# Performance work log

Measured on AMD Instinct MI355X. Metric: run time of the kernel, lower is better.

## Reference

```python
import jax, jax.numpy as jnp
import numpy as np
from jax import lax

NPOINT = 2048
RADIUS = 0.1
NSAMPLE = 32


def setup_inputs() -> dict:
    key = jax.random.key(0)
    ks = jax.random.split(key, 6)
    B, N, C = 8, 16384, 16
    xyz = jax.random.uniform(ks[0], (B, N, 3), dtype=jnp.float32)
    features = jax.random.normal(ks[1], (B, N, C), dtype=jnp.float32)
    W1 = jax.random.normal(ks[2], (C, 32), dtype=jnp.float32) * 0.1
    b1 = jnp.zeros((32,), jnp.float32)
    W2 = jax.random.normal(ks[3], (32, 32), dtype=jnp.float32) * 0.1
    b2 = jnp.zeros((32,), jnp.float32)
    W3 = jax.random.normal(ks[4], (32, 64), dtype=jnp.float32) * 0.1
    b3 = jnp.zeros((64,), jnp.float32)
    return {"xyz": xyz, "features": features,
            "W1": W1, "b1": b1, "W2": W2, "b2": b2, "W3": W3, "b3": b3}


def farthest_point_sample(xyz, npoint):
    # Sequential FPS: keep running min-distance to selected set, argmax each step.
    B, N, _ = xyz.shape

    def step(carry, _):
        min_d, far = carry  # min_d: [B,N], far: [B]
        centroid = jnp.take_along_axis(xyz, far[:, None, None], axis=1)  # [B,1,3]
        d = jnp.sum((xyz - centroid) ** 2, axis=-1)                      # [B,N]
        min_d = jnp.minimum(min_d, d)
        nxt = jnp.argmax(min_d, axis=1).astype(jnp.int32)
        return (min_d, nxt), far

    init = (jnp.full((B, N), 1e10, xyz.dtype), jnp.zeros((B,), jnp.int32))
    _, idx = lax.scan(step, init, None, length=npoint)  # idx: [npoint, B]
    return idx.T  # [B, npoint]


def ball_query(radius, nsample, xyz, new_xyz):
    # Squared pairwise distances [B, S, N]
    d2 = (jnp.sum(new_xyz ** 2, -1)[:, :, None]
          + jnp.sum(xyz ** 2, -1)[:, None, :]
          - 2.0 * jnp.einsum('bsd,bnd->bsn', new_xyz, xyz))
    N = xyz.shape[1]
    # Take the first `nsample` in-ball indices (by point order), pad with first found.
    scores = jnp.where(d2 <= radius * radius,
                       jnp.arange(N, dtype=jnp.int32), jnp.int32(N))
    vals = -lax.top_k(-scores, nsample)[0]  # smallest nsample scores, ascending
    first = vals[..., :1]                   # center itself is always in-ball
    return jnp.where(vals == N, first, vals)  # [B, S, nsample] int32


def reference(xyz, features, W1, b1, W2, b2, W3, b3):
    fps_idx = farthest_point_sample(xyz, NPOINT)                      # [B,S]
    new_xyz = jnp.take_along_axis(xyz, fps_idx[..., None], axis=1)    # [B,S,3]
    idx = ball_query(RADIUS, NSAMPLE, xyz, new_xyz)                   # [B,S,K]
    grouped = jax.vmap(lambda f, i: f[i])(features, idx)              # [B,S,K,C]
    h = jax.nn.relu(grouped @ W1 + b1)
    h = jax.nn.relu(h @ W2 + b2)
    h = h @ W3 + b3                                                   # [B,S,K,64]
    new_features = jnp.max(h, axis=2)                                 # [B,S,64]
    return new_xyz, new_features
```

## Files before the change

kernel.cpp:

```cpp
#include <hip/hip_runtime.h>

#define B 8
#define N 16384
#define S 2048
#define NS 32
#define CIN 16
#define NCELL 4096

typedef float f32x2 __attribute__((ext_vector_type(2)));
typedef int   i32x2 __attribute__((ext_vector_type(2)));
typedef unsigned long long u64;

template<int CTRL>
__device__ __forceinline__ float dpp_fmax(float x) {
    int t = __builtin_amdgcn_update_dpp(0, __float_as_int(x), CTRL, 0xF, 0xF, true);
    return fmaxf(x, __int_as_float(t));
}
template<int CTRL>
__device__ __forceinline__ unsigned dpp_umax(unsigned x) {
    unsigned t = (unsigned)__builtin_amdgcn_update_dpp(0, (int)x, CTRL, 0xF, 0xF, true);
    return x > t ? x : t;
}
__device__ __forceinline__ float wave_fmax(float x) {
    x = dpp_fmax<0xB1>(x);
    x = dpp_fmax<0x4E>(x);
    x = dpp_fmax<0x114>(x);
    x = dpp_fmax<0x118>(x);
    x = dpp_fmax<0x142>(x);
    x = dpp_fmax<0x143>(x);
    return __int_as_float(__builtin_amdgcn_readlane(__float_as_int(x), 63));
}
__device__ __forceinline__ unsigned wave_umax(unsigned x) {
    x = dpp_umax<0xB1>(x);
    x = dpp_umax<0x4E>(x);
    x = dpp_umax<0x114>(x);
    x = dpp_umax<0x118>(x);
    x = dpp_umax<0x142>(x);
    x = dpp_umax<0x143>(x);
    return (unsigned)__builtin_amdgcn_readlane((int)x, 63);
}

__device__ __forceinline__ int expand4(int v) {
    return (v & 1) | ((v & 2) << 2) | ((v & 4) << 4) | ((v & 8) << 6);
}

__global__ __launch_bounds__(1024) void bucket_kernel(const float* __restrict__ xyz,
                                                      float* __restrict__ Xp,
                                                      float* __restrict__ Yp,
                                                      float* __restrict__ Zp,
                                                      int* __restrict__ Ip) {
    const int b = blockIdx.x;
    const int t = threadIdx.x;
    const float* xb = xyz + (size_t)b * N * 3;

    __shared__ int hist[NCELL];
    __shared__ int run[NCELL];
    __shared__ int pA[1024], pB[1024];
    for (int i = t; i < NCELL; i += 1024) { hist[i] = 0; run[i] = 0; }
    __syncthreads();

    int cell[16];
    float xs[16], ys[16], zs[16];
#pragma unroll
    for (int k = 0; k < 16; ++k) {
        const int n = t + (k << 10);
        const float x = xb[3 * n + 0];
        const float y = xb[3 * n + 1];
        const float z = xb[3 * n + 2];
        const int cx = min(15, max(0, (int)(x * 16.0f)));
        const int cy = min(15, max(0, (int)(y * 16.0f)));
        const int cz = min(15, max(0, (int)(z * 16.0f)));
        const int c = expand4(cx) | (expand4(cy) << 1) | (expand4(cz) << 2);
        cell[k] = c; xs[k] = x; ys[k] = y; zs[k] = z;
        atomicAdd(&hist[c], 1);
    }
    __syncthreads();

    const int h0 = hist[4 * t + 0], h1 = hist[4 * t + 1],
              h2 = hist[4 * t + 2], h3 = hist[4 * t + 3];
    const int lsum = h0 + h1 + h2 + h3;
    pA[t] = lsum;
    __syncthreads();
    int* cur = pA; int* nxt = pB;
    for (int off = 1; off < 1024; off <<= 1) {
        nxt[t] = cur[t] + ((t >= off) ? cur[t - off] : 0);
        __syncthreads();
        int* tmp = cur; cur = nxt; nxt = tmp;
    }
    const int excl = cur[t] - lsum;
    __syncthreads();
    hist[4 * t + 0] = excl;
    hist[4 * t + 1] = excl + h0;
    hist[4 * t + 2] = excl + h0 + h1;
    hist[4 * t + 3] = excl + h0 + h1 + h2;
    __syncthreads();

#pragma unroll
    for (int k = 0; k < 16; ++k) {
        const int c = cell[k];
        const int pos = hist[c] + atomicAdd(&run[c], 1);
        const size_t o = (size_t)b * N + pos;
        Xp[o] = xs[k]; Yp[o] = ys[k]; Zp[o] = zs[k];
        Ip[o] = t + (k << 10);
    }
}

__global__ __launch_bounds__(1024, 1) void fps_prune_kernel(const float* __restrict__ xyz,
                                                            const float* __restrict__ Xp,
                                                            const float* __restrict__ Yp,
                                                            const float* __restrict__ Zp,
                                                            const int* __restrict__ Ip,
                                                            float* __restrict__ new_xyz) {
#pragma clang fp contract(off)
    const int b = blockIdx.x;
    const int t = threadIdx.x;
    const float* xb = xyz + (size_t)b * N * 3;
    const size_t base = (size_t)b * N + ((size_t)t << 4);

    f32x2 px[8], py[8], pz[8], md[8];
    i32x2 ip[8];
    {
        const f32x2* X2 = (const f32x2*)(Xp + base);
        const f32x2* Y2 = (const f32x2*)(Yp + base);
        const f32x2* Z2 = (const f32x2*)(Zp + base);
        const i32x2* I2 = (const i32x2*)(Ip + base);
#pragma unroll
        for (int j = 0; j < 8; ++j) {
            px[j] = X2[j]; py[j] = Y2[j]; pz[j] = Z2[j]; ip[j] = I2[j];
            md[j] = (f32x2){1e10f, 1e10f};
        }
    }

    float lox = px[0].x, hix = px[0].x, loy = py[0].x, hiy = py[0].x,
          loz = pz[0].x, hiz = pz[0].x;
#pragma unroll
    for (int j = 0; j < 8; ++j) {
        lox = fminf(lox, fminf(px[j].x, px[j].y)); hix = fmaxf(hix, fmaxf(px[j].x, px[j].y));
        loy = fminf(loy, fminf(py[j].x, py[j].y)); hiy = fmaxf(hiy, fmaxf(py[j].x, py[j].y));
        loz = fminf(loz, fminf(pz[j].x, pz[j].y)); hiz = fmaxf(hiz, fmaxf(pz[j].x, pz[j].y));
    }

    __shared__ u64 slotp[4];
    if (t == 0) { slotp[0] = 0ull; slotp[1] = 0ull; slotp[2] = 0ull; slotp[3] = 0ull; }
    __syncthreads();

    int p = 0;
    float ub = 1e10f;
    int cand = ip[0].x;
    u64 wkey = 0ull;
    float cx = xb[0], cy = xb[1], cz = xb[2];

    for (int it = 0; it < S; ++it) {
        if (t == 0) {
            float* o = new_xyz + ((size_t)b * S + it) * 3;
            o[0] = cx; o[1] = cy; o[2] = cz;
        }
        const float ddx = fmaxf(0.0f, fmaxf(lox - cx, cx - hix));
        const float ddy = fmaxf(0.0f, fmaxf(loy - cy, cy - hiy));
        const float ddz = fmaxf(0.0f, fmaxf(loz - cz, cz - hiz));
        const float lb = (ddx * ddx + ddy * ddy) + ddz * ddz;
        const bool upd = !(lb * 0.99998f > ub);

        if (__any(upd)) {
            if (upd) {
                asm volatile("" : "+v"(px[0]), "+v"(px[1]), "+v"(px[2]), "+v"(px[3]),
                                  "+v"(px[4]), "+v"(px[5]), "+v"(px[6]), "+v"(px[7]));
                asm volatile("" : "+v"(py[0]), "+v"(py[1]), "+v"(py[2]), "+v"(py[3]),
                                  "+v"(py[4]), "+v"(py[5]), "+v"(py[6]), "+v"(py[7]));
                asm volatile("" : "+v"(pz[0]), "+v"(pz[1]), "+v"(pz[2]), "+v"(pz[3]),
                                  "+v"(pz[4]), "+v"(pz[5]), "+v"(pz[6]), "+v"(pz[7]));
                asm volatile("" : "+v"(ip[0]), "+v"(ip[1]), "+v"(ip[2]), "+v"(ip[3]),
                                  "+v"(ip[4]), "+v"(ip[5]), "+v"(ip[6]), "+v"(ip[7]));
                const f32x2 c2x = {cx, cx}, c2y = {cy, cy}, c2z = {cz, cz};
                f32x2 nu2 = {0.0f, 0.0f};
#pragma unroll
                for (int j = 0; j < 8; ++j) {
                    const f32x2 dx = px[j] - c2x;
                    const f32x2 dy = py[j] - c2y;
                    const f32x2 dz = pz[j] - c2z;
                    const f32x2 dd = (dx * dx + dy * dy) + dz * dz;
                    const f32x2 m = __builtin_elementwise_min(md[j], dd);
                    md[j] = m;
                    nu2 = __builtin_elementwise_max(nu2, m);
                }
                const float nu = fmaxf(nu2.x, nu2.y);
                int c = 0x7fffffff;
#pragma unroll
                for (int j = 0; j < 8; ++j) {
                    if (md[j].x == nu) c = min(c, ip[j].x);
                    if (md[j].y == nu) c = min(c, ip[j].y);
                }
                ub = nu; cand = c;
            }
            const float wmax = wave_fmax(ub);
            unsigned cn = (ub == wmax) ? ~(unsigned)cand : 0u;
            cn = wave_umax(cn);
            wkey = ((u64)__float_as_uint(wmax) << 32) | (u64)cn;
        }
        if ((t & 63) == 0) atomicMax(&slotp[p], wkey);
        const int pn = (p + 1) & 3;
        if (t == 0) slotp[pn] = 0ull;
        __syncthreads();
        const u64 r = slotp[p];
        const int fu = __builtin_amdgcn_readfirstlane((int)(~(unsigned)r));
        cx = xb[3 * fu + 0];
        cy = xb[3 * fu + 1];
        cz = xb[3 * fu + 2];
        p = pn;
    }
}

__global__ __launch_bounds__(1024) void fps_kernel(const float* __restrict__ xyz,
                                                   float* __restrict__ new_xyz) {
#pragma clang fp contract(off)
    const int b = blockIdx.x;
    const int t = threadIdx.x;
    const float* xb = xyz + (size_t)b * N * 3;

    float px[16], py[16], pz[16], md[16];
#pragma unroll
    for (int k = 0; k < 16; ++k) {
        const int n = t + (k << 10);
        px[k] = xb[3 * n + 0];
        py[k] = xb[3 * n + 1];
        pz[k] = xb[3 * n + 2];
        md[k] = 1e10f;
    }
    __shared__ float rv[2][16];
    __shared__ int slot[2];
    if (t == 0) { slot[0] = 0x7fffffff; slot[1] = 0x7fffffff; }
    __syncthreads();
    int far = 0, p = 0;
    const int lane = t & 63, w = t >> 6;
    for (int it = 0; it < S; ++it) {
        const float cx = xb[3 * far + 0], cy = xb[3 * far + 1], cz = xb[3 * far + 2];
        if (t == 0) {
            float* o = new_xyz + ((size_t)b * S + it) * 3;
            o[0] = cx; o[1] = cy; o[2] = cz;
        }
        float bestv = -1.0f;
#pragma unroll
        for (int k = 0; k < 16; ++k) {
            const float dx = __fsub_rn(px[k], cx);
            const float dy = __fsub_rn(py[k], cy);
            const float dz = __fsub_rn(pz[k], cz);
            const float d  = __fadd_rn(__fadd_rn(__fmul_rn(dx, dx), __fmul_rn(dy, dy)),
                                       __fmul_rn(dz, dz));
            const float m = fminf(md[k], d);
            md[k] = m;
            bestv = fmaxf(bestv, m);
        }
        float v = bestv;
#pragma unroll
        for (int off = 32; off >= 1; off >>= 1) v = fmaxf(v, __shfl_xor(v, off));
        if (lane == 0) rv[p][w] = v;
        __syncthreads();
        float u = rv[p][lane & 15];
#pragma unroll
        for (int off = 8; off >= 1; off >>= 1) u = fmaxf(u, __shfl_xor(u, off));
        if (t == 0) slot[p ^ 1] = 0x7fffffff;
        if (bestv == u) {
            int cnd2 = 0x7fffffff;
#pragma unroll
            for (int k = 0; k < 16; ++k)
                if (md[k] == u) cnd2 = min(cnd2, t + (k << 10));
            atomicMin(&slot[p], cnd2);
        }
        __syncthreads();
        far = slot[p];
        p ^= 1;
    }
}

__global__ __launch_bounds__(64) void ball_mlp_kernel(
    const float* __restrict__ xyz,
    const float* __restrict__ feat,
    const float* __restrict__ W1, const float* __restrict__ b1,
    const float* __restrict__ W2, const float* __restrict__ b2,
    const float* __restrict__ W3, const float* __restrict__ b3,
    const float* __restrict__ new_xyz,
    float* __restrict__ out_feat) {
#pragma clang fp contract(off)
    const int q = blockIdx.x;
    const int b = q >> 11;
    const int lane = threadIdx.x;
    const float* xb = xyz + (size_t)b * N * 3;

    const double qx = (double)new_xyz[3 * q + 0];
    const double qy = (double)new_xyz[3 * q + 1];
    const double qz = (double)new_xyz[3 * q + 2];
    const double s2 = qx * qx + qy * qy + qz * qz;
    const double R2 = 0.1 * 0.1;

    __shared__ int idxbuf[NS];
    int found = 0;
    for (int bs = 0; bs < N; bs += 64) {
        const int n = bs + lane;
        const double x = (double)xb[3 * n + 0];
        const double y = (double)xb[3 * n + 1];
        const double z = (double)xb[3 * n + 2];
        const double n2 = x * x + y * y + z * z;
        const double dt = qx * x + qy * y + qz * z;
        const double d2 = (s2 + n2) - 2.0 * dt;
        const bool ok = (d2 <= R2);
        const unsigned long long msk = __ballot(ok);
        if (ok) {
            const int pos = found + (int)__popcll(msk & ((1ull << lane) - 1ull));
            if (pos < NS) idxbuf[pos] = n;
        }
        found += (int)__popcll(msk);
        if (found >= NS) break;
    }
    __syncthreads();
    if (lane == 0) {
        const int cnt = found < NS ? found : NS;
        const int first = (cnt > 0) ? idxbuf[0] : (N - 1);
        for (int j2 = cnt; j2 < NS; ++j2) idxbuf[j2] = first;
    }
    __syncthreads();

    const int j = lane & 31;
    const int h = lane >> 5;
    const int nid = idxbuf[j];
    const float* fp = feat + ((size_t)b * N + nid) * CIN;
    float fv[CIN];
#pragma unroll
    for (int k = 0; k < CIN; ++k) fv[k] = fp[k];

    float h1[32];
#pragma unroll
    for (int c = 0; c < 32; ++c) {
        float a = b1[c];
#pragma unroll
        for (int k = 0; k < CIN; ++k) a = fmaf(fv[k], W1[(k << 5) + c], a);
        h1[c] = fmaxf(a, 0.0f);
    }
    float h2[32];
#pragma unroll
    for (int c = 0; c < 32; ++c) {
        float a = b2[c];
#pragma unroll
        for (int k = 0; k < 32; ++k) a = fmaf(h1[k], W2[(k << 5) + c], a);
        h2[c] = fmaxf(a, 0.0f);
    }
    const int cbase = h << 5;
    float mx[32];
#pragma unroll
    for (int c = 0; c < 32; ++c) {
        float a = b3[cbase + c];
#pragma unroll
        for (int k = 0; k < 32; ++k) a = fmaf(h2[k], W3[(k << 6) + cbase + c], a);
        mx[c] = a;
    }
#pragma unroll
    for (int off = 1; off <= 16; off <<= 1) {
#pragma unroll
        for (int c = 0; c < 32; ++c) mx[c] = fmaxf(mx[c], __shfl_xor(mx[c], off));
    }
    if (j == 0) {
        float* o = out_feat + (size_t)q * 64 + cbase;
#pragma unroll
        for (int c = 0; c < 32; ++c) o[c] = mx[c];
    }
}

extern "C" void kernel_launch(void* const* d_in, const int* in_sizes, int n_in,
                              void* d_out, int out_size, void* d_ws, size_t ws_size,
                              hipStream_t stream) {
    (void)in_sizes; (void)n_in; (void)out_size;
    const float* xyz  = (const float*)d_in[0];
    const float* feat = (const float*)d_in[1];
    const float* W1   = (const float*)d_in[2];
    const float* b1   = (const float*)d_in[3];
    const float* W2   = (const float*)d_in[4];
    const float* b2   = (const float*)d_in[5];
    const float* W3   = (const float*)d_in[6];
    const float* b3   = (const float*)d_in[7];

    float* out      = (float*)d_out;
    float* new_xyz  = out;
    float* new_feat = out + (size_t)B * S * 3;

    const size_t need = (size_t)4 * B * N * sizeof(float);
    if (ws_size >= need) {
        float* Xp = (float*)d_ws;
        float* Yp = Xp + (size_t)B * N;
        float* Zp = Yp + (size_t)B * N;
        int*   Ip = (int*)(Zp + (size_t)B * N);
        bucket_kernel<<<B, 1024, 0, stream>>>(xyz, Xp, Yp, Zp, Ip);
        fps_prune_kernel<<<B, 1024, 0, stream>>>(xyz, Xp, Yp, Zp, Ip, new_xyz);
    } else {
        fps_kernel<<<B, 1024, 0, stream>>>(xyz, new_xyz);
    }
    ball_mlp_kernel<<<B * S, 64, 0, stream>>>(xyz, feat, W1, b1, W2, b2, W3, b3,
                                              new_xyz, new_feat);
}
```

Measured before the change: 2.437 ms.

## Use spatial cell buckets for ball query instead of linear point scan

Bucket kernel now exports per-cell start offsets, and a new ball-query kernel scans only the coarse grid cells overlapping the query sphere. It collects all in-ball candidates, then selects the smallest 32 original indices to match first-by-index semantics. This replaces a long linear scan over points per query with a small local search, at the cost of extra workspace and a selection step when more than 32 candidates are found.

```diff
diff --git a/kernel.cpp b/kernel.cpp
--- a/kernel.cpp
+++ b/kernel.cpp
@@ -6,6 +6,7 @@
 #define NS 32
 #define CIN 16
 #define NCELL 4096
+#define CCAP 512
 
 typedef float f32x2 __attribute__((ext_vector_type(2)));
 typedef int   i32x2 __attribute__((ext_vector_type(2)));
@@ -48,10 +49,12 @@
                                                       float* __restrict__ Xp,
                                                       float* __restrict__ Yp,
                                                       float* __restrict__ Zp,
-                                                      int* __restrict__ Ip) {
+                                                      int* __restrict__ Ip,
+                                                      int* __restrict__ starts) {
     const int b = blockIdx.x;
     const int t = threadIdx.x;
     const float* xb = xyz + (size_t)b * N * 3;
+    int* st = starts + (size_t)b * (NCELL + 1);
 
     __shared__ int hist[NCELL];
     __shared__ int run[NCELL];
@@ -94,6 +97,9 @@
     hist[4 * t + 2] = excl + h0 + h1;
     hist[4 * t + 3] = excl + h0 + h1 + h2;
     __syncthreads();
+
+    for (int i = t; i < NCELL; i += 1024) st[i] = hist[i];
+    if (t == 0) st[NCELL] = N;
 
 #pragma unroll
     for (int k = 0; k < 16; ++k) {
@@ -270,6 +276,169 @@
         far = slot[p];
         p ^= 1;
     }
+}
+
+__device__ __forceinline__ void mlp_tail(const float* __restrict__ feat,
+                                         const float* __restrict__ W1, const float* __restrict__ b1,
+                                         const float* __restrict__ W2, const float* __restrict__ b2,
+                                         const float* __restrict__ W3, const float* __restrict__ b3,
+                                         const int* sel, int b, int q, int lane,
+                                         float* __restrict__ out_feat) {
+    const int j = lane & 31;
+    const int h = lane >> 5;
+    const int nid = sel[j];
+    const float* fp = feat + ((size_t)b * N + nid) * CIN;
+    float fv[CIN];
+#pragma unroll
+    for (int k = 0; k < CIN; ++k) fv[k] = fp[k];
+
+    float h1[32];
+#pragma unroll
+    for (int c = 0; c < 32; ++c) {
+        float a = b1[c];
+#pragma unroll
+        for (int k = 0; k < CIN; ++k) a = fmaf(fv[k], W1[(k << 5) + c], a);
+        h1[c] = fmaxf(a, 0.0f);
+    }
+    float h2[32];
+#pragma unroll
+    for (int c = 0; c < 32; ++c) {
+        float a = b2[c];
+#pragma unroll
+        for (int k = 0; k < 32; ++k) a = fmaf(h1[k], W2[(k << 5) + c], a);
+        h2[c] = fmaxf(a, 0.0f);
+    }
+    const int cbase = h << 5;
+    float mx[32];
+#pragma unroll
+    for (int c = 0; c < 32; ++c) {
+        float a = b3[cbase + c];
+#pragma unroll
+        for (int k = 0; k < 32; ++k) a = fmaf(h2[k], W3[(k << 6) + cbase + c], a);
+        mx[c] = a;
+    }
+#pragma unroll
+    for (int off = 1; off <= 16; off <<= 1) {
+#pragma unroll
+        for (int c = 0; c < 32; ++c) mx[c] = fmaxf(mx[c], __shfl_xor(mx[c], off));
+    }
+    if (j == 0) {
+        float* o = out_feat + (size_t)q * 64 + cbase;
+#pragma unroll
+        for (int c = 0; c < 32; ++c) o[c] = mx[c];
+    }
+}
+
+__global__ __launch_bounds__(64) void ball_mlp_cells_kernel(
+    const float* __restrict__ feat,
+    const float* __restrict__ W1, const float* __restrict__ b1,
+    const float* __restrict__ W2, const float* __restrict__ b2,
+    const float* __restrict__ W3, const float* __restrict__ b3,
+    const float* __restrict__ new_xyz,
+    const float* __restrict__ Xp, const float* __restrict__ Yp,
+    const float* __restrict__ Zp, const int* __restrict__ Ip,
+    const int* __restrict__ starts,
+    float* __restrict__ out_feat) {
+#pragma clang fp contract(off)
+    const int q = blockIdx.x;
+    const int b = q >> 11;
+    const int lane = threadIdx.x;
+    const size_t bn = (size_t)b * N;
+
+    const double qx = (double)new_xyz[3 * q + 0];
+    const double qy = (double)new_xyz[3 * q + 1];
+    const double qz = (double)new_xyz[3 * q + 2];
+    const double s2 = qx * qx + qy * qy + qz * qz;
+    const double R2 = 0.1 * 0.1;
+
+    const int axl = min(7, max(0, (int)floor((qx - 0.1 - 2e-5) * 8.0)));
+    const int axh = min(7, max(0, (int)floor((qx + 0.1 + 2e-5) * 8.0)));
+    const int ayl = min(7, max(0, (int)floor((qy - 0.1 - 2e-5) * 8.0)));
+    const int ayh = min(7, max(0, (int)floor((qy + 0.1 + 2e-5) * 8.0)));
+    const int azl = min(7, max(0, (int)floor((qz - 0.1 - 2e-5) * 8.0)));
+    const int azh = min(7, max(0, (int)floor((qz + 0.1 + 2e-5) * 8.0)));
+    const int nx = axh - axl + 1, ny = ayh - ayl + 1, nz = azh - azl + 1;
+    const int ncell = nx * ny * nz;
+
+    int s_ = 0, e_ = 0;
+    if (lane < ncell) {
+        const int lx = lane % nx;
+        const int rr = lane / nx;
+        const int ly = rr % ny;
+        const int lz = rr / ny;
+        const int code8 = expand4(axl + lx) | (expand4(ayl + ly) << 1)
+                        | (expand4(azl + lz) << 2);
+        const int* stp = starts + (size_t)b * (NCELL + 1) + (code8 << 3);
+        s_ = stp[0];
+        e_ = stp[8];
+    }
+
+    __shared__ int cbuf[CCAP];
+    int cnt = 0;
+    for (int c = 0; c < ncell; ++c) {
+        const int cs = __shfl(s_, c);
+        const int ce = __shfl(e_, c);
+        for (int ii = cs; ii < ce; ii += 64) {
+            const int i = ii + lane;
+            const bool act = i < ce;
+            const int ig = act ? i : cs;
+            const double x = (double)Xp[bn + ig];
+            const double y = (double)Yp[bn + ig];
+            const double z = (double)Zp[bn + ig];
+            const double n2 = x * x + y * y + z * z;
+            const double dt = qx * x + qy * y + qz * z;
+            const double d2 = (s2 + n2) - 2.0 * dt;
+            const bool ok = act && (d2 <= R2);
+            const unsigned long long msk = __ballot(ok);
+            if (ok) {
+                const int pos = cnt + (int)__popcll(msk & ((1ull << lane) - 1ull));
+                if (pos < CCAP) cbuf[pos] = Ip[bn + ig];
+            }
+            cnt += (int)__popcll(msk);
+        }
+    }
+    if (cnt > CCAP) cnt = CCAP;
+    __syncthreads();
+
+    __shared__ int sel[NS];
+    int myc[8];
+#pragma unroll
+    for (int r = 0; r < 8; ++r) {
+        const int idx = lane + (r << 6);
+        myc[r] = (idx < cnt) ? cbuf[idx] : 0x7fffffff;
+    }
+    const int nsel = cnt < NS ? cnt : NS;
+    if (cnt <= NS) {
+#pragma unroll
+        for (int r = 0; r < 8; ++r) {
+            const int idx = lane + (r << 6);
+            if (idx < cnt) sel[idx] = myc[r];
+        }
+    } else {
+        for (int k = 0; k < NS; ++k) {
+            int lm = myc[0];
+#pragma unroll
+            for (int r = 1; r < 8; ++r) lm = min(lm, myc[r]);
+            const int wm = (int)~wave_umax(~(unsigned)lm);
+            if (lane == 0) sel[k] = wm;
+#pragma unroll
+            for (int r = 0; r < 8; ++r) if (myc[r] == wm) myc[r] = 0x7fffffff;
+        }
+    }
+    __syncthreads();
+    if (lane == 0) {
+        int first;
+        if (nsel > 0) {
+            first = sel[0];
+            for (int k = 1; k < nsel; ++k) first = min(first, sel[k]);
+        } else {
+            first = N - 1;
+        }
+        for (int k = nsel; k < NS; ++k) sel[k] = first;
+    }
+    __syncthreads();
+
+    mlp_tail(feat, W1, b1, W2, b2, W3, b3, sel, b, q, lane, out_feat);
 }
 
 __global__ __launch_bounds__(64) void ball_mlp_kernel(
@@ -318,50 +487,7 @@
         for (int j2 = cnt; j2 < NS; ++j2) idxbuf[j2] = first;
     }
     __syncthreads();
-
-    const int j = lane & 31;
-    const int h = lane >> 5;
-    const int nid = idxbuf[j];
-    const float* fp = feat + ((size_t)b * N + nid) * CIN;
-    float fv[CIN];
-#pragma unroll
-    for (int k = 0; k < CIN; ++k) fv[k] = fp[k];
-
-    float h1[32];
-#pragma unroll
-    for (int c = 0; c < 32; ++c) {
-        float a = b1[c];
-#pragma unroll
-        for (int k = 0; k < CIN; ++k) a = fmaf(fv[k], W1[(k << 5) + c], a);
-        h1[c] = fmaxf(a, 0.0f);
-    }
-    float h2[32];
-#pragma unroll
-    for (int c = 0; c < 32; ++c) {
-        float a = b2[c];
-#pragma unroll
-        for (int k = 0; k < 32; ++k) a = fmaf(h1[k], W2[(k << 5) + c], a);
-        h2[c] = fmaxf(a, 0.0f);
-    }
-    const int cbase = h << 5;
-    float mx[32];
-#pragma unroll
-    for (int c = 0; c < 32; ++c) {
-        float a = b3[cbase + c];
-#pragma unroll
-        for (int k = 0; k < 32; ++k) a = fmaf(h2[k], W3[(k << 6) + cbase + c], a);
-        mx[c] = a;
-    }
-#pragma unroll
-    for (int off = 1; off <= 16; off <<= 1) {
-#pragma unroll
-        for (int c = 0; c < 32; ++c) mx[c] = fmaxf(mx[c], __shfl_xor(mx[c], off));
-    }
-    if (j == 0) {
-        float* o = out_feat + (size_t)q * 64 + cbase;
-#pragma unroll
-        for (int c = 0; c < 32; ++c) o[c] = mx[c];
-    }
+    mlp_tail(feat, W1, b1, W2, b2, W3, b3, idxbuf, b, q, lane, out_feat);
 }
 
 extern "C" void kernel_launch(void* const* d_in, const int* in_sizes, int n_in,
@@ -381,17 +507,22 @@
     float* new_xyz  = out;
     float* new_feat = out + (size_t)B * S * 3;
 
-    const size_t need = (size_t)4 * B * N * sizeof(float);
+    const size_t need = (size_t)4 * B * N * sizeof(float)
+                      + (size_t)B * (NCELL + 1) * sizeof(int);
     if (ws_size >= need) {
         float* Xp = (float*)d_ws;
         float* Yp = Xp + (size_t)B * N;
         float* Zp = Yp + (size_t)B * N;
         int*   Ip = (int*)(Zp + (size_t)B * N);
-        bucket_kernel<<<B, 1024, 0, stream>>>(xyz, Xp, Yp, Zp, Ip);
+        int*   St = Ip + (size_t)B * N;
+        bucket_kernel<<<B, 1024, 0, stream>>>(xyz, Xp, Yp, Zp, Ip, St);
         fps_prune_kernel<<<B, 1024, 0, stream>>>(xyz, Xp, Yp, Zp, Ip, new_xyz);
+        ball_mlp_cells_kernel<<<B * S, 64, 0, stream>>>(feat, W1, b1, W2, b2, W3, b3,
+                                                        new_xyz, Xp, Yp, Zp, Ip, St,
+                                                        new_feat);
     } else {
         fps_kernel<<<B, 1024, 0, stream>>>(xyz, new_xyz);
-    }
-    ball_mlp_kernel<<<B * S, 64, 0, stream>>>(xyz, feat, W1, b1, W2, b2, W3, b3,
-                                              new_xyz, new_feat);
-}
+        ball_mlp_kernel<<<B * S, 64, 0, stream>>>(xyz, feat, W1, b1, W2, b2, W3, b3,
+                                                  new_xyz, new_feat);
+    }
+}
```

Measured after the change: 2.253 ms. 7.5% less time.
